# Kernel optimization log

Hardware: AMD Instinct MI355X
Metric: run time of the kernel (lower is better)

Reference implementation:

```python
import jax, jax.numpy as jnp
import numpy as np


def _xnor_quant_weight(w):
    # XnorBinaryLinear.quant_weight: row-center, sign-binarize, scale by
    # per-output-channel mean absolute value (STE in training; forward value
    # is sign(wc) * scale).
    wc = w - jnp.mean(w, axis=1, keepdims=True)          # [OC, IC]
    scale = jnp.mean(jnp.abs(wc), axis=1, keepdims=True)  # [OC, 1]
    return jnp.sign(wc) * scale


def setup_inputs() -> dict:
    key = jax.random.key(0)
    k1, k2, k3, k4 = jax.random.split(key, 4)
    OC = IC = 4096
    N_OUT = int(0.05 * IC)  # 204 outlier columns
    TOKENS = 4096
    x = jax.random.normal(k1, (TOKENS, IC), dtype=jnp.float32)
    weight = jax.random.normal(k2, (OC, IC), dtype=jnp.float32) * 0.02
    bias = jax.random.normal(k3, (OC,), dtype=jnp.float32) * 0.02
    outlier_weight = jax.random.normal(k4, (OC, N_OUT), dtype=jnp.float32) * 0.02
    outlier_columns_index = jnp.arange(N_OUT, dtype=jnp.int32)
    return {
        "x": x,
        "weight": weight,
        "bias": bias,
        "outlier_weight": outlier_weight,
        "outlier_columns_index": outlier_columns_index,
    }


def reference(x, weight, bias, outlier_weight, outlier_columns_index):
    # binarize_except_outliers: quantize dense weight, then overwrite the
    # outlier input-channel columns with the kept full-precision weights.
    wq = _xnor_quant_weight(weight)                      # [OC, IC]
    wq = wq.at[:, outlier_columns_index].set(outlier_weight)
    # F.linear(x, w, b) = x @ w.T + b
    return jnp.einsum("ti,oi->to", x, wq) + bias
```

## Files before the change

### kernel.cpp

```cpp
#include <hip/hip_runtime.h>

typedef __bf16 bf16;
typedef __bf16 bf16x8 __attribute__((ext_vector_type(8)));
typedef float  f32x4  __attribute__((ext_vector_type(4)));
typedef int    i32x4  __attribute__((ext_vector_type(4)));
typedef signed char i8;

#define OC_N   4096
#define IC_K   4096
#define TOKENS 4096
#define KC     256

__global__ __launch_bounds__(256) void prep_kernel(
    const float* __restrict__ w, const float* __restrict__ x,
    const float* __restrict__ ow, const int* __restrict__ idx,
    i8* __restrict__ wsgn, i8* __restrict__ xq,
    bf16* __restrict__ xo, bf16* __restrict__ wcorr,
    float* __restrict__ scale_arr, float* __restrict__ sx_arr, int n_out)
{
    __shared__ float red[8];
    const int row = blockIdx.x;
    const int t = threadIdx.x;
    const int lane = t & 63, wv = t >> 6;

    const float4* wr = (const float4*)(w + (size_t)row * IC_K);
    float4 v[4];
    float s = 0.f;
#pragma unroll
    for (int i = 0; i < 4; i++) {
        v[i] = wr[i * 256 + t];
        s += v[i].x + v[i].y + v[i].z + v[i].w;
    }
    for (int o = 32; o > 0; o >>= 1) s += __shfl_down(s, o, 64);
    if (lane == 0) red[wv] = s;
    __syncthreads();
    const float mean = (red[0] + red[1] + red[2] + red[3]) * (1.f / IC_K);

    float sa = 0.f;
#pragma unroll
    for (int i = 0; i < 4; i++) {
        sa += fabsf(v[i].x - mean) + fabsf(v[i].y - mean) +
              fabsf(v[i].z - mean) + fabsf(v[i].w - mean);
    }
    for (int o = 32; o > 0; o >>= 1) sa += __shfl_down(sa, o, 64);
    if (lane == 0) red[4 + wv] = sa;
    __syncthreads();
    const float scale = (red[4] + red[5] + red[6] + red[7]) * (1.f / IC_K);

    i8* srow = wsgn + (size_t)row * IC_K;
#pragma unroll
    for (int i = 0; i < 4; i++) {
        float c[4] = { v[i].x - mean, v[i].y - mean, v[i].z - mean, v[i].w - mean };
        char4 q;
        q.x = (i8)((c[0] > 0.f) - (c[0] < 0.f));
        q.y = (i8)((c[1] > 0.f) - (c[1] < 0.f));
        q.z = (i8)((c[2] > 0.f) - (c[2] < 0.f));
        q.w = (i8)((c[3] > 0.f) - (c[3] < 0.f));
        *(char4*)(srow + (size_t)(i * 256 + t) * 4) = q;
    }

    const float4* xr = (const float4*)(x + (size_t)row * IC_K);
    float4 u[4];
    float mx = 0.f;
#pragma unroll
    for (int i = 0; i < 4; i++) {
        u[i] = xr[i * 256 + t];
        mx = fmaxf(mx, fmaxf(fmaxf(fabsf(u[i].x), fabsf(u[i].y)),
                             fmaxf(fabsf(u[i].z), fabsf(u[i].w))));
    }
    for (int o = 32; o > 0; o >>= 1) mx = fmaxf(mx, __shfl_down(mx, o, 64));
    if (lane == 0) red[wv] = mx;
    __syncthreads();
    const float maxv = fmaxf(fmaxf(red[0], red[1]), fmaxf(red[2], red[3]));
    const float inv = maxv > 0.f ? 127.f / maxv : 0.f;
    const float sxv = maxv > 0.f ? maxv * (1.f / 127.f) : 1.f;

    i8* xrow = xq + (size_t)row * IC_K;
#pragma unroll
    for (int i = 0; i < 4; i++) {
        char4 q;
        q.x = (i8)(int)rintf(u[i].x * inv);
        q.y = (i8)(int)rintf(u[i].y * inv);
        q.z = (i8)(int)rintf(u[i].z * inv);
        q.w = (i8)(int)rintf(u[i].w * inv);
        *(char4*)(xrow + (size_t)(i * 256 + t) * 4) = q;
    }
    if (t == 0) { scale_arr[row] = scale; sx_arr[row] = sxv; }

    if (t < n_out) {
        const int col = idx[t];
        xo[(size_t)row * KC + t] = (bf16)x[(size_t)row * IC_K + col];
        const float wc_ = w[(size_t)row * IC_K + col] - mean;
        const float sg = (wc_ > 0.f) ? 1.f : ((wc_ < 0.f) ? -1.f : 0.f);
        wcorr[(size_t)row * KC + t] = (bf16)(ow[(size_t)row * n_out + t] - scale * sg);
    } else if (t < KC) {
        xo[(size_t)row * KC + t] = (bf16)0.f;
        wcorr[(size_t)row * KC + t] = (bf16)0.f;
    }
}

__device__ __forceinline__ void gload16(const void* g, void* l)
{
    __builtin_amdgcn_global_load_lds(
        (const __attribute__((address_space(1))) void*)g,
        (__attribute__((address_space(3))) void*)l, 16, 0, 0);
}

__global__ __launch_bounds__(256) void gemm_kernel(
    const i8* __restrict__ A, const i8* __restrict__ B,
    const bf16* __restrict__ Axo, const bf16* __restrict__ Bwc,
    const float* __restrict__ sx, const float* __restrict__ scale,
    const float* __restrict__ bias, float* __restrict__ C)
{
    constexpr int K = IC_K, N = OC_N, BK = 128, TM = 128, TN = 128;
    __shared__ __align__(16) i8 As[TM * BK];
    __shared__ __align__(16) i8 Bs[TN * BK];

    const int bm = blockIdx.y, bn = blockIdx.x;
    const int tid = threadIdx.x, lane = tid & 63, wave = tid >> 6;
    const int wm = wave >> 1, wn = wave & 1;

    const int srow = lane >> 3;
    const int soct = (lane & 7) ^ srow;
    const i8* ga = A + (size_t)(bm * TM + wave * 32 + srow) * K + soct * 16;
    const i8* gb = B + (size_t)(bn * TN + wave * 32 + srow) * K + soct * 16;
    i8* lA = &As[wave * 32 * BK];
    i8* lB = &Bs[wave * 32 * BK];
    const int rxor = lane & 7;

    i32x4 acc[4][4] = {};

    for (int k0 = 0; k0 < K; k0 += BK) {
#pragma unroll
        for (int i = 0; i < 4; i++) {
            gload16(ga + k0 + (size_t)(i * 8) * K, lA + i * 8 * BK);
            gload16(gb + k0 + (size_t)(i * 8) * K, lB + i * 8 * BK);
        }
        __syncthreads();

#pragma unroll
        for (int s = 0; s < 2; s++) {
            const int lq = s * 4 + (lane >> 4);
            const int pq = lq ^ rxor;
            i32x4 af[4], bfr[4];
#pragma unroll
            for (int i = 0; i < 4; i++)
                af[i] = *(const i32x4*)&As[(wm * 64 + i * 16 + (lane & 15)) * BK + pq * 16];
#pragma unroll
            for (int i = 0; i < 4; i++)
                bfr[i] = *(const i32x4*)&Bs[(wn * 64 + i * 16 + (lane & 15)) * BK + pq * 16];
#pragma unroll
            for (int mi = 0; mi < 4; mi++)
#pragma unroll
                for (int ni = 0; ni < 4; ni++)
                    acc[mi][ni] = __builtin_amdgcn_mfma_i32_16x16x64_i8(
                        af[mi], bfr[ni], acc[mi][ni], 0, 0, 0);
        }
        __syncthreads();
    }

    const int col0 = bn * TN + wn * 64 + (lane & 15);
    const int row0 = bm * TM + wm * 64 + (lane >> 4) * 4;
    float scl[4];
#pragma unroll
    for (int ni = 0; ni < 4; ni++) scl[ni] = scale[col0 + ni * 16];
    f32x4 facc[4][4];
#pragma unroll
    for (int mi = 0; mi < 4; mi++) {
        float sxv[4];
#pragma unroll
        for (int r = 0; r < 4; r++) sxv[r] = sx[row0 + mi * 16 + r];
#pragma unroll
        for (int ni = 0; ni < 4; ni++)
#pragma unroll
            for (int r = 0; r < 4; r++)
                facc[mi][ni][r] = (float)acc[mi][ni][r] * sxv[r] * scl[ni];
    }

    bf16* As2 = (bf16*)As;
    bf16* Bs2 = (bf16*)Bs;
    const bf16* ga2 = Axo + (size_t)(bm * TM + wave * 32 + srow) * KC + soct * 8;
    const bf16* gb2 = Bwc + (size_t)(bn * TN + wave * 32 + srow) * KC + soct * 8;
    bf16* lA2 = As2 + wave * 32 * 64;
    bf16* lB2 = Bs2 + wave * 32 * 64;

    for (int k0 = 0; k0 < KC; k0 += 64) {
#pragma unroll
        for (int i = 0; i < 4; i++) {
            gload16(ga2 + k0 + (size_t)(i * 8) * KC, lA2 + i * 8 * 64);
            gload16(gb2 + k0 + (size_t)(i * 8) * KC, lB2 + i * 8 * 64);
        }
        __syncthreads();

#pragma unroll
        for (int s = 0; s < 2; s++) {
            const int lq = s * 4 + (lane >> 4);
            const int pq = lq ^ rxor;
            bf16x8 af2[4], bf2[4];
#pragma unroll
            for (int i = 0; i < 4; i++)
                af2[i] = *(const bf16x8*)&As2[(wave >> 1) * 0 + (wm * 64 + i * 16 + (lane & 15)) * 64 + pq * 8];
#pragma unroll
            for (int i = 0; i < 4; i++)
                bf2[i] = *(const bf16x8*)&Bs2[(wn * 64 + i * 16 + (lane & 15)) * 64 + pq * 8];
#pragma unroll
            for (int mi = 0; mi < 4; mi++)
#pragma unroll
                for (int ni = 0; ni < 4; ni++)
                    facc[mi][ni] = __builtin_amdgcn_mfma_f32_16x16x32_bf16(
                        af2[mi], bf2[ni], facc[mi][ni], 0, 0, 0);
        }
        __syncthreads();
    }

#pragma unroll
    for (int ni = 0; ni < 4; ni++) {
        const float bv = bias[col0 + ni * 16];
#pragma unroll
        for (int mi = 0; mi < 4; mi++) {
#pragma unroll
            for (int r = 0; r < 4; r++) {
                C[(size_t)(row0 + mi * 16 + r) * N + col0 + ni * 16] =
                    facc[mi][ni][r] + bv;
            }
        }
    }
}

extern "C" void kernel_launch(void* const* d_in, const int* in_sizes, int n_in,
                              void* d_out, int out_size, void* d_ws, size_t ws_size,
                              hipStream_t stream)
{
    const float* x    = (const float*)d_in[0];
    const float* w    = (const float*)d_in[1];
    const float* bias = (const float*)d_in[2];
    const float* ow   = (const float*)d_in[3];
    const int*   idx  = (const int*)d_in[4];
    const int    n_out = in_sizes[4];
    float* out = (float*)d_out;

    char* ws = (char*)d_ws;
    i8*    xq    = (i8*)ws;
    i8*    wsgn  = (i8*)(ws + (size_t)16 * 1024 * 1024);
    bf16*  xo    = (bf16*)(ws + (size_t)32 * 1024 * 1024);
    bf16*  wcorr = (bf16*)(ws + (size_t)34 * 1024 * 1024);
    float* sx    = (float*)(ws + (size_t)36 * 1024 * 1024);
    float* scl   = (float*)(ws + (size_t)36 * 1024 * 1024 + 16 * 1024);

    hipLaunchKernelGGL(prep_kernel, dim3(OC_N), dim3(256), 0, stream,
                       w, x, ow, idx, wsgn, xq, xo, wcorr, scl, sx, n_out);
    hipLaunchKernelGGL(gemm_kernel, dim3(OC_N / 128, TOKENS / 128), dim3(256),
                       0, stream, xq, wsgn, xo, wcorr, sx, scl, bias, out);
}
```

Baseline: 258.3 us.

## Switch GEMM to 32x32 MFMA tiles with reworked LDS swizzle

Replaces the 16x16x64 int8 and 16x16x32 bf16 MFMA instructions with their 32x32 variants (32x32x32 i8, 32x32x16 bf16). Each wave now holds a 2x2 grid of 32x32 accumulators instead of 4x4 16x16 ones, which halves the LDS fragment loads per MFMA. The LDS XOR swizzle is rewritten to fit the new fragment access pattern and avoid bank conflicts, and the epilogue is remapped to the 32x32 output layout. The 32x32 instructions have longer latency per issue, so throughput depends on whether the scheduler can keep them overlapped.

```diff
diff --git a/kernel.cpp b/kernel.cpp
--- a/kernel.cpp
+++ b/kernel.cpp
@@ -3,7 +3,9 @@
 typedef __bf16 bf16;
 typedef __bf16 bf16x8 __attribute__((ext_vector_type(8)));
 typedef float  f32x4  __attribute__((ext_vector_type(4)));
+typedef float  f32x16 __attribute__((ext_vector_type(16)));
 typedef int    i32x4  __attribute__((ext_vector_type(4)));
+typedef int    i32x16 __attribute__((ext_vector_type(16)));
 typedef signed char i8;
 
 #define OC_N   4096
@@ -121,108 +123,107 @@
     const int wm = wave >> 1, wn = wave & 1;
 
     const int srow = lane >> 3;
-    const int soct = (lane & 7) ^ srow;
-    const i8* ga = A + (size_t)(bm * TM + wave * 32 + srow) * K + soct * 16;
-    const i8* gb = B + (size_t)(bn * TN + wave * 32 + srow) * K + soct * 16;
+    const int q0 = (lane & 7) ^ srow ^ ((wave & 1) * 4);
+    const i8* ga = A + (size_t)(bm * TM + wave * 32 + srow) * K;
+    const i8* gb = B + (size_t)(bn * TN + wave * 32 + srow) * K;
     i8* lA = &As[wave * 32 * BK];
     i8* lB = &Bs[wave * 32 * BK];
-    const int rxor = lane & 7;
-
-    i32x4 acc[4][4] = {};
+
+    const int kg = lane >> 5;
+    const int m32 = lane & 31;
+    const int frb = (lane & 7) ^ ((lane >> 3) & 3);
+
+    i32x16 acc[2][2] = {};
 
     for (int k0 = 0; k0 < K; k0 += BK) {
 #pragma unroll
         for (int i = 0; i < 4; i++) {
-            gload16(ga + k0 + (size_t)(i * 8) * K, lA + i * 8 * BK);
-            gload16(gb + k0 + (size_t)(i * 8) * K, lB + i * 8 * BK);
-        }
-        __syncthreads();
-
-#pragma unroll
-        for (int s = 0; s < 2; s++) {
-            const int lq = s * 4 + (lane >> 4);
-            const int pq = lq ^ rxor;
-            i32x4 af[4], bfr[4];
-#pragma unroll
-            for (int i = 0; i < 4; i++)
-                af[i] = *(const i32x4*)&As[(wm * 64 + i * 16 + (lane & 15)) * BK + pq * 16];
-#pragma unroll
-            for (int i = 0; i < 4; i++)
-                bfr[i] = *(const i32x4*)&Bs[(wn * 64 + i * 16 + (lane & 15)) * BK + pq * 16];
-#pragma unroll
-            for (int mi = 0; mi < 4; mi++)
-#pragma unroll
-                for (int ni = 0; ni < 4; ni++)
-                    acc[mi][ni] = __builtin_amdgcn_mfma_i32_16x16x64_i8(
+            gload16(ga + k0 + (size_t)(i * 8) * K + (q0 ^ i) * 16, lA + i * 8 * BK);
+            gload16(gb + k0 + (size_t)(i * 8) * K + (q0 ^ i) * 16, lB + i * 8 * BK);
+        }
+        __syncthreads();
+
+#pragma unroll
+        for (int t = 0; t < 4; t++) {
+            i32x4 af[2], bfr[2];
+#pragma unroll
+            for (int ti = 0; ti < 2; ti++) {
+                const int pq = ((t << 1) | kg) ^ frb ^ (ti << 2);
+                af[ti]  = *(const i32x4*)&As[(wm * 64 + ti * 32 + m32) * BK + pq * 16];
+                bfr[ti] = *(const i32x4*)&Bs[(wn * 64 + ti * 32 + m32) * BK + pq * 16];
+            }
+#pragma unroll
+            for (int mi = 0; mi < 2; mi++)
+#pragma unroll
+                for (int ni = 0; ni < 2; ni++)
+                    acc[mi][ni] = __builtin_amdgcn_mfma_i32_32x32x32_i8(
                         af[mi], bfr[ni], acc[mi][ni], 0, 0, 0);
         }
         __syncthreads();
     }
 
-    const int col0 = bn * TN + wn * 64 + (lane & 15);
-    const int row0 = bm * TM + wm * 64 + (lane >> 4) * 4;
-    float scl[4];
-#pragma unroll
-    for (int ni = 0; ni < 4; ni++) scl[ni] = scale[col0 + ni * 16];
-    f32x4 facc[4][4];
-#pragma unroll
-    for (int mi = 0; mi < 4; mi++) {
-        float sxv[4];
-#pragma unroll
-        for (int r = 0; r < 4; r++) sxv[r] = sx[row0 + mi * 16 + r];
-#pragma unroll
-        for (int ni = 0; ni < 4; ni++)
-#pragma unroll
-            for (int r = 0; r < 4; r++)
-                facc[mi][ni][r] = (float)acc[mi][ni][r] * sxv[r] * scl[ni];
+    const int col0 = bn * TN + wn * 64 + m32;
+    const int rbase = bm * TM + wm * 64 + 4 * kg;
+    float scl2[2], bv[2];
+#pragma unroll
+    for (int ni = 0; ni < 2; ni++) {
+        scl2[ni] = scale[col0 + ni * 32];
+        bv[ni]   = bias[col0 + ni * 32];
+    }
+    f32x16 facc[2][2];
+#pragma unroll
+    for (int mi = 0; mi < 2; mi++) {
+#pragma unroll
+        for (int reg = 0; reg < 16; reg++) {
+            const float sxv = sx[rbase + mi * 32 + (reg & 3) + 8 * (reg >> 2)];
+#pragma unroll
+            for (int ni = 0; ni < 2; ni++)
+                facc[mi][ni][reg] = (float)acc[mi][ni][reg] * sxv * scl2[ni];
+        }
     }
 
     bf16* As2 = (bf16*)As;
     bf16* Bs2 = (bf16*)Bs;
-    const bf16* ga2 = Axo + (size_t)(bm * TM + wave * 32 + srow) * KC + soct * 8;
-    const bf16* gb2 = Bwc + (size_t)(bn * TN + wave * 32 + srow) * KC + soct * 8;
+    const bf16* ga2 = Axo + (size_t)(bm * TM + wave * 32 + srow) * KC;
+    const bf16* gb2 = Bwc + (size_t)(bn * TN + wave * 32 + srow) * KC;
     bf16* lA2 = As2 + wave * 32 * 64;
     bf16* lB2 = Bs2 + wave * 32 * 64;
 
     for (int k0 = 0; k0 < KC; k0 += 64) {
 #pragma unroll
         for (int i = 0; i < 4; i++) {
-            gload16(ga2 + k0 + (size_t)(i * 8) * KC, lA2 + i * 8 * 64);
-            gload16(gb2 + k0 + (size_t)(i * 8) * KC, lB2 + i * 8 * 64);
-        }
-        __syncthreads();
-
-#pragma unroll
-        for (int s = 0; s < 2; s++) {
-            const int lq = s * 4 + (lane >> 4);
-            const int pq = lq ^ rxor;
-            bf16x8 af2[4], bf2[4];
-#pragma unroll
-            for (int i = 0; i < 4; i++)
-                af2[i] = *(const bf16x8*)&As2[(wave >> 1) * 0 + (wm * 64 + i * 16 + (lane & 15)) * 64 + pq * 8];
-#pragma unroll
-            for (int i = 0; i < 4; i++)
-                bf2[i] = *(const bf16x8*)&Bs2[(wn * 64 + i * 16 + (lane & 15)) * 64 + pq * 8];
-#pragma unroll
-            for (int mi = 0; mi < 4; mi++)
-#pragma unroll
-                for (int ni = 0; ni < 4; ni++)
-                    facc[mi][ni] = __builtin_amdgcn_mfma_f32_16x16x32_bf16(
+            gload16(ga2 + k0 + (size_t)(i * 8) * KC + (q0 ^ i) * 8, lA2 + i * 8 * 64);
+            gload16(gb2 + k0 + (size_t)(i * 8) * KC + (q0 ^ i) * 8, lB2 + i * 8 * 64);
+        }
+        __syncthreads();
+
+#pragma unroll
+        for (int t = 0; t < 4; t++) {
+            bf16x8 af2[2], bf2[2];
+#pragma unroll
+            for (int ti = 0; ti < 2; ti++) {
+                const int pq = ((t << 1) | kg) ^ frb ^ (ti << 2);
+                af2[ti] = *(const bf16x8*)&As2[(wm * 64 + ti * 32 + m32) * 64 + pq * 8];
+                bf2[ti] = *(const bf16x8*)&Bs2[(wn * 64 + ti * 32 + m32) * 64 + pq * 8];
+            }
+#pragma unroll
+            for (int mi = 0; mi < 2; mi++)
+#pragma unroll
+                for (int ni = 0; ni < 2; ni++)
+                    facc[mi][ni] = __builtin_amdgcn_mfma_f32_32x32x16_bf16(
                         af2[mi], bf2[ni], facc[mi][ni], 0, 0, 0);
         }
         __syncthreads();
     }
 
 #pragma unroll
-    for (int ni = 0; ni < 4; ni++) {
-        const float bv = bias[col0 + ni * 16];
-#pragma unroll
-        for (int mi = 0; mi < 4; mi++) {
-#pragma unroll
-            for (int r = 0; r < 4; r++) {
-                C[(size_t)(row0 + mi * 16 + r) * N + col0 + ni * 16] =
-                    facc[mi][ni][r] + bv;
-            }
+    for (int mi = 0; mi < 2; mi++) {
+#pragma unroll
+        for (int reg = 0; reg < 16; reg++) {
+            const int row = rbase + mi * 32 + (reg & 3) + 8 * (reg >> 2);
+#pragma unroll
+            for (int ni = 0; ni < 2; ni++)
+                C[(size_t)row * N + col0 + ni * 32] = facc[mi][ni][reg] + bv[ni];
         }
     }
 }
```

After: 256.3 us. About the same (-0.8%).
